# Optimization experiments

Hardware: AMD Instinct MI355X
Metric: run time of the kernel (lower is better)

## Reference

```python
import jax, jax.numpy as jnp
import numpy as np

N = 2_000_000           # agents
T = 10                  # timesteps
G_HOUSEHOLD = 800_000   # groups per edge type
G_COMPANY = 20_000
G_SCHOOL = 65_000
TAU = 0.1               # gumbel-softmax temperature (GradABM-JUNE default)


def setup_inputs() -> dict:
    key = jax.random.key(0)
    ks = jax.random.split(key, 6)
    # pre-sampled standard Gumbel noise for the differentiable Bernoulli sampling
    u = jax.random.uniform(ks[0], (T, 2, N), minval=1e-9, maxval=1.0)
    gumbel = (-jnp.log(-jnp.log(u))).astype(jnp.float32)
    return {
        "beta_parameters": jnp.array([0.3, 0.2, 0.4], dtype=jnp.float32),
        "transmissions": 0.1 * jax.random.uniform(ks[1], (N,), dtype=jnp.float32),
        "susceptibilities": jnp.ones((N,), dtype=jnp.float32),
        "gumbel": gumbel,
        "g_household": jax.random.randint(ks[2], (N,), 0, G_HOUSEHOLD),
        "g_company": jax.random.randint(ks[3], (N,), 0, G_COMPANY),
        "g_school": jax.random.randint(ks[4], (N,), 0, G_SCHOOL),
        "n_timesteps": T,
    }


def _infection_step(betas, transm, susc, gumbel_t, group_ids, group_sizes):
    """One InfectionPassing forward + gumbel-softmax sampling."""
    trans_susc = jnp.zeros_like(transm)
    for beta, gids, G in zip(betas, group_ids, group_sizes):
        # group sizes -> contact probability (constant wrt params)
        people = jax.ops.segment_sum(jnp.ones_like(transm), gids, num_segments=G)
        p_contact = jax.lax.stop_gradient(jnp.minimum(1.0 / (people - 1.0), 1.0))
        # agent -> group scatter-add of transmissions, weighted by beta * p_contact
        cum_trans = beta * p_contact * jax.ops.segment_sum(transm, gids, num_segments=G)
        # group -> agent gather, weighted by susceptibility
        trans_susc = trans_susc + cum_trans[gids] * susc
    not_infected = jnp.exp(-trans_susc)
    # hard (straight-through) gumbel-softmax Bernoulli sample, class 1 = infected
    logits = jnp.log(jnp.clip(jnp.stack([not_infected, 1.0 - not_infected]), 1e-15))  # [2, N]
    y = jax.nn.softmax((logits + gumbel_t) / TAU, axis=0)
    hard = jax.nn.one_hot(jnp.argmax(y, axis=0), 2, axis=0, dtype=y.dtype)
    sample = hard + y - jax.lax.stop_gradient(y)
    return sample[1]


def reference(beta_parameters, transmissions, susceptibilities, gumbel,
              g_household, g_company, g_school, n_timesteps):
    group_ids = (g_household, g_company, g_school)
    group_sizes = (G_HOUSEHOLD, G_COMPANY, G_SCHOOL)
    betas = (beta_parameters[0], beta_parameters[1], beta_parameters[2])

    def scan_fn(carry, gumbel_t):
        transm, susc = carry
        new_inf = _infection_step(betas, transm, susc, gumbel_t, group_ids, group_sizes)
        return (transm + 0.2 * new_inf, susc - new_inf), new_inf

    _, ret = jax.lax.scan(scan_fn, (transmissions, susceptibilities), gumbel[:n_timesteps])
    return ret  # [T, N] stacked new_infected per timestep (vstack equivalent)
```

## Files before the change

### kernel.cpp

```cpp
#include <hip/hip_runtime.h>

#define NAGENTS 2000000
#define GH 800000
#define GC 20000
#define GS 65000
#define GT (GH + GC + GS)
#define TSTEPS 10
#define NXCD 8

#define FIXD   17592186044416.0
#define INVFIX (1.0 / 17592186044416.0)
#define DELTA  3518437208883ULL
#define CUNIT  (1ULL << 51)
#define SMASK  (CUNIT - 1ULL)

#define SUSCBIT (1ULL << 63)

__global__ void init_pack_repl_kernel(const float* __restrict__ transm_in,
                                      const float* __restrict__ susc_in,
                                      const int* __restrict__ gh,
                                      const int* __restrict__ gc,
                                      const int* __restrict__ gs,
                                      unsigned long long* __restrict__ repl,
                                      unsigned long long* __restrict__ packed,
                                      int n) {
    int i = blockIdx.x * blockDim.x + threadIdx.x;
    if (i >= n) return;

    unsigned xcd;
    asm volatile("s_getreg_b32 %0, hwreg(HW_REG_XCC_ID)" : "=s"(xcd));
    unsigned long long* myrep = repl + (size_t)(xcd & (NXCD - 1)) * GT;

    int a = __builtin_nontemporal_load(&gh[i]);
    int b = __builtin_nontemporal_load(&gc[i]);
    int c = __builtin_nontemporal_load(&gs[i]);
    float sv = __builtin_nontemporal_load(&susc_in[i]);
    float tv = __builtin_nontemporal_load(&transm_in[i]);

    unsigned long long w = (unsigned long long)(unsigned)a
                         | ((unsigned long long)(unsigned)b << 20)
                         | ((unsigned long long)(unsigned)c << 35)
                         | (sv != 0.0f ? SUSCBIT : 0ULL);
    __builtin_nontemporal_store(w, &packed[i]);

    unsigned long long e =
        (unsigned long long)((double)tv * FIXD + 0.5) + CUNIT;
    __hip_atomic_fetch_add(&myrep[a], e, __ATOMIC_RELAXED,
                           __HIP_MEMORY_SCOPE_WORKGROUP);
    __hip_atomic_fetch_add(&myrep[GH + b], e, __ATOMIC_RELAXED,
                           __HIP_MEMORY_SCOPE_WORKGROUP);
    __hip_atomic_fetch_add(&myrep[GH + GC + c], e, __ATOMIC_RELAXED,
                           __HIP_MEMORY_SCOPE_WORKGROUP);
}

__global__ void combine_from_repl_kernel(const float* __restrict__ betas,
                                         const unsigned long long* __restrict__ repl,
                                         unsigned long long* __restrict__ buf,
                                         float* __restrict__ cur, int ntot) {
    int g = blockIdx.x * blockDim.x + threadIdx.x;
    if (g >= ntot) return;
    unsigned long long v = 0;
#pragma unroll
    for (int x = 0; x < NXCD; ++x)
        v += __builtin_nontemporal_load(&repl[(size_t)x * GT + g]);
    buf[g] = v;
    float people = (float)(v >> 51);
    float p = fminf(1.0f / (people - 1.0f), 1.0f);
    float beta = (g < GH) ? betas[0] : (g < GH + GC) ? betas[1] : betas[2];
    float sum = (float)((double)(long long)(v & SMASK) * INVFIX);
    cur[g] = (beta * p) * sum;
}

__global__ void combine_kernel(const float* __restrict__ betas,
                               const unsigned long long* __restrict__ buf,
                               float* __restrict__ cur, int ntot) {
    int g = blockIdx.x * blockDim.x + threadIdx.x;
    if (g >= ntot) return;
    unsigned long long v = __builtin_nontemporal_load(&buf[g]);
    float people = (float)(v >> 51);
    float p = fminf(1.0f / (people - 1.0f), 1.0f);
    float beta = (g < GH) ? betas[0] : (g < GH + GC) ? betas[1] : betas[2];
    float sum = (float)((double)(long long)(v & SMASK) * INVFIX);
    cur[g] = (beta * p) * sum;
}

template <bool LAST>
__global__ void step_packed_kernel(const float* __restrict__ gum_t,
                                   unsigned long long* __restrict__ packed,
                                   const float* __restrict__ cur,
                                   unsigned long long* __restrict__ buf,
                                   float* __restrict__ out_t,
                                   int n) {
    int i = blockIdx.x * blockDim.x + threadIdx.x;
    if (i >= n) return;

    unsigned long long w = __builtin_nontemporal_load(&packed[i]);
    float ninf = 0.0f;
    if (w & SUSCBIT) {
        int a = (int)(w & 0xFFFFFULL);
        int b = GH + (int)((w >> 20) & 0x7FFFULL);
        int c = GH + GC + (int)((w >> 35) & 0x1FFFFULL);
        float ts = cur[a];
        ts += cur[b];
        ts += cur[c];

        float ni = expf(-ts);
        float l0 = logf(fmaxf(ni, 1e-15f));
        float l1 = logf(fmaxf(1.0f - ni, 1e-15f));
        float g0 = __builtin_nontemporal_load(&gum_t[i]);
        float g1 = __builtin_nontemporal_load(&gum_t[(size_t)n + i]);
        float z0 = (l0 + g0) / 0.1f;
        float z1 = (l1 + g1) / 0.1f;
        if (z1 > z0) {
            ninf = 1.0f;
            if (!LAST) {
                packed[i] = w & ~SUSCBIT;
                atomicAdd(&buf[a], DELTA);
                atomicAdd(&buf[b], DELTA);
                atomicAdd(&buf[c], DELTA);
            }
        }
    }
    __builtin_nontemporal_store(ninf, &out_t[i]);
}

__global__ void init_pack_kernel(const float* __restrict__ transm_in,
                                 const float* __restrict__ susc_in,
                                 const int* __restrict__ gh,
                                 const int* __restrict__ gc,
                                 const int* __restrict__ gs,
                                 unsigned long long* __restrict__ buf,
                                 unsigned long long* __restrict__ packed,
                                 int n) {
    int i = blockIdx.x * blockDim.x + threadIdx.x;
    if (i >= n) return;
    int a = __builtin_nontemporal_load(&gh[i]);
    int b = __builtin_nontemporal_load(&gc[i]);
    int c = __builtin_nontemporal_load(&gs[i]);
    float sv = __builtin_nontemporal_load(&susc_in[i]);
    float tv = __builtin_nontemporal_load(&transm_in[i]);

    unsigned long long w = (unsigned long long)(unsigned)a
                         | ((unsigned long long)(unsigned)b << 20)
                         | ((unsigned long long)(unsigned)c << 35)
                         | (sv != 0.0f ? SUSCBIT : 0ULL);
    __builtin_nontemporal_store(w, &packed[i]);

    unsigned long long e =
        (unsigned long long)((double)tv * FIXD + 0.5) + CUNIT;
    atomicAdd(&buf[a], e);
    atomicAdd(&buf[GH + b], e);
    atomicAdd(&buf[GH + GC + c], e);
}

extern "C" void kernel_launch(void* const* d_in, const int* in_sizes, int n_in,
                              void* d_out, int out_size, void* d_ws, size_t ws_size,
                              hipStream_t stream) {
    const float* betas     = (const float*)d_in[0];
    const float* transm_in = (const float*)d_in[1];
    float*       susc      = (float*)d_in[2];
    const float* gumbel    = (const float*)d_in[3];
    const int*   gh        = (const int*)d_in[4];
    const int*   gc        = (const int*)d_in[5];
    const int*   gs        = (const int*)d_in[6];
    int          n         = in_sizes[1];
    float*       out       = (float*)d_out;

    unsigned long long* buf = (unsigned long long*)d_ws;
    float* cur = (float*)((char*)d_ws + (size_t)GT * 8);
    size_t packOff = ((size_t)GT * 12 + 255) & ~(size_t)255;
    unsigned long long* packed =
        (unsigned long long*)((char*)d_ws + packOff);
    size_t replOff = (packOff + (size_t)n * 8 + 255) & ~(size_t)255;
    unsigned long long* repl =
        (unsigned long long*)((char*)d_ws + replOff);
    size_t need_repl = replOff + (size_t)NXCD * GT * 8;
    size_t need_pack = packOff + (size_t)n * 8;

    const int blk = 256;
    const int grid_n = (n + blk - 1) / blk;
    const int grid_g = (GT + blk - 1) / blk;

    if (ws_size >= need_repl) {
        hipMemsetAsync(repl, 0, (size_t)NXCD * GT * 8, stream);
        init_pack_repl_kernel<<<grid_n, blk, 0, stream>>>(
            transm_in, susc, gh, gc, gs, repl, packed, n);
        for (int t = 0; t < TSTEPS; ++t) {
            const float* gum_t = gumbel + (size_t)2 * t * n;
            float* out_t = out + (size_t)t * n;
            if (t == 0) {
                combine_from_repl_kernel<<<grid_g, blk, 0, stream>>>(
                    betas, repl, buf, cur, GT);
            } else {
                combine_kernel<<<grid_g, blk, 0, stream>>>(betas, buf, cur, GT);
            }
            if (t == TSTEPS - 1) {
                step_packed_kernel<true><<<grid_n, blk, 0, stream>>>(
                    gum_t, packed, cur, buf, out_t, n);
            } else {
                step_packed_kernel<false><<<grid_n, blk, 0, stream>>>(
                    gum_t, packed, cur, buf, out_t, n);
            }
        }
        return;
    }

    hipMemsetAsync(buf, 0, (size_t)GT * 8, stream);
    if (ws_size >= need_pack) {
        init_pack_kernel<<<grid_n, blk, 0, stream>>>(
            transm_in, susc, gh, gc, gs, buf, packed, n);
        for (int t = 0; t < TSTEPS; ++t) {
            const float* gum_t = gumbel + (size_t)2 * t * n;
            float* out_t = out + (size_t)t * n;
            combine_kernel<<<grid_g, blk, 0, stream>>>(betas, buf, cur, GT);
            if (t == TSTEPS - 1) {
                step_packed_kernel<true><<<grid_n, blk, 0, stream>>>(
                    gum_t, packed, cur, buf, out_t, n);
            } else {
                step_packed_kernel<false><<<grid_n, blk, 0, stream>>>(
                    gum_t, packed, cur, buf, out_t, n);
            }
        }
    }
}
```

Before: 984.1 us.

## Replace per-XCD atomic scatter with binned counting-sort segment reduction

The initial group-sum scatter now uses a two-pass counting sort instead of per-XCD replicated global atomics. Agents are histogrammed into group-range bins per block, the histogram is prefix-scanned, (group, transmission) pairs are scattered into bins, and each bin is reduced with shared-memory atomics. The aim is to replace random global 64-bit atomics with LDS atomics and more local writes. The cost is extra passes, a 3N-entry binned buffer, several more kernel launches, and scatter writes with poor coalescing.

```diff
diff --git a/kernel.cpp b/kernel.cpp
--- a/kernel.cpp
+++ b/kernel.cpp
@@ -1,4 +1,6 @@
 #include <hip/hip_runtime.h>
+
+typedef unsigned long long u64;
 
 #define NAGENTS 2000000
 #define GH 800000
@@ -6,7 +8,6 @@
 #define GS 65000
 #define GT (GH + GC + GS)
 #define TSTEPS 10
-#define NXCD 8
 
 #define FIXD   17592186044416.0
 #define INVFIX (1.0 / 17592186044416.0)
@@ -16,54 +17,131 @@
 
 #define SUSCBIT (1ULL << 63)
 
-__global__ void init_pack_repl_kernel(const float* __restrict__ transm_in,
-                                      const float* __restrict__ susc_in,
-                                      const int* __restrict__ gh,
-                                      const int* __restrict__ gc,
-                                      const int* __restrict__ gs,
-                                      unsigned long long* __restrict__ repl,
-                                      unsigned long long* __restrict__ packed,
-                                      int n) {
-    int i = blockIdx.x * blockDim.x + threadIdx.x;
-    if (i >= n) return;
-
-    unsigned xcd;
-    asm volatile("s_getreg_b32 %0, hwreg(HW_REG_XCC_ID)" : "=s"(xcd));
-    unsigned long long* myrep = repl + (size_t)(xcd & (NXCD - 1)) * GT;
-
-    int a = __builtin_nontemporal_load(&gh[i]);
-    int b = __builtin_nontemporal_load(&gc[i]);
-    int c = __builtin_nontemporal_load(&gs[i]);
-    float sv = __builtin_nontemporal_load(&susc_in[i]);
-    float tv = __builtin_nontemporal_load(&transm_in[i]);
-
-    unsigned long long w = (unsigned long long)(unsigned)a
-                         | ((unsigned long long)(unsigned)b << 20)
-                         | ((unsigned long long)(unsigned)c << 35)
-                         | (sv != 0.0f ? SUSCBIT : 0ULL);
-    __builtin_nontemporal_store(w, &packed[i]);
-
-    unsigned long long e =
-        (unsigned long long)((double)tv * FIXD + 0.5) + CUNIT;
-    __hip_atomic_fetch_add(&myrep[a], e, __ATOMIC_RELAXED,
-                           __HIP_MEMORY_SCOPE_WORKGROUP);
-    __hip_atomic_fetch_add(&myrep[GH + b], e, __ATOMIC_RELAXED,
-                           __HIP_MEMORY_SCOPE_WORKGROUP);
-    __hip_atomic_fetch_add(&myrep[GH + GC + c], e, __ATOMIC_RELAXED,
-                           __HIP_MEMORY_SCOPE_WORKGROUP);
-}
-
-__global__ void combine_from_repl_kernel(const float* __restrict__ betas,
-                                         const unsigned long long* __restrict__ repl,
-                                         unsigned long long* __restrict__ buf,
-                                         float* __restrict__ cur, int ntot) {
+#define NB_H 3125
+#define NB_C 2500
+#define NB_S 2032
+#define NBINS (NB_H + NB_C + NB_S)
+#define NBP 256
+#define P12_THR 512
+#define SCAN_ELEMS 2048
+
+__device__ __forceinline__ int bin_h(int a) { return a >> 8; }
+__device__ __forceinline__ int bin_c(int c) { return NB_H + (c >> 3); }
+__device__ __forceinline__ int bin_s(int s) { return NB_H + NB_C + (s >> 5); }
+
+__global__ __launch_bounds__(P12_THR) void p1_hist_pack(
+    const int* __restrict__ gh, const int* __restrict__ gc,
+    const int* __restrict__ gs, const float* __restrict__ susc_in,
+    u64* __restrict__ packed, unsigned* __restrict__ hist,
+    int n, int apb) {
+    __shared__ unsigned h[NBINS];
+    for (int j = threadIdx.x; j < NBINS; j += P12_THR) h[j] = 0;
+    __syncthreads();
+    const int b = blockIdx.x;
+    const int lo = b * apb, hi = min(n, lo + apb);
+    for (int i = lo + threadIdx.x; i < hi; i += P12_THR) {
+        int a = gh[i], c = gc[i], s = gs[i];
+        float sv = susc_in[i];
+        u64 w = (u64)(unsigned)a | ((u64)(unsigned)c << 20)
+              | ((u64)(unsigned)s << 35) | (sv != 0.0f ? SUSCBIT : 0ULL);
+        __builtin_nontemporal_store(w, &packed[i]);
+        atomicAdd(&h[bin_h(a)], 1u);
+        atomicAdd(&h[bin_c(c)], 1u);
+        atomicAdd(&h[bin_s(s)], 1u);
+    }
+    __syncthreads();
+    for (int j = threadIdx.x; j < NBINS; j += P12_THR)
+        hist[(size_t)j * NBP + b] = h[j];
+}
+
+__global__ __launch_bounds__(1024) void s1_scan(unsigned* __restrict__ data,
+                                                unsigned* __restrict__ sums,
+                                                int ntot) {
+    __shared__ unsigned sA[1024], sB[1024];
+    const int base = blockIdx.x * SCAN_ELEMS;
+    const int t = threadIdx.x;
+    unsigned v0 = (base + 2 * t     < ntot) ? data[base + 2 * t]     : 0u;
+    unsigned v1 = (base + 2 * t + 1 < ntot) ? data[base + 2 * t + 1] : 0u;
+    sA[t] = v0 + v1;
+    __syncthreads();
+    unsigned* src = sA; unsigned* dst = sB;
+    for (int off = 1; off < 1024; off <<= 1) {
+        dst[t] = src[t] + (t >= off ? src[t - off] : 0u);
+        __syncthreads();
+        unsigned* tmp = src; src = dst; dst = tmp;
+    }
+    unsigned incl = src[t];
+    unsigned expair = incl - (v0 + v1);
+    if (base + 2 * t     < ntot) data[base + 2 * t]     = expair;
+    if (base + 2 * t + 1 < ntot) data[base + 2 * t + 1] = expair + v0;
+    if (t == 1023) sums[blockIdx.x] = incl;
+}
+
+__global__ __launch_bounds__(1024) void s3_add(unsigned* __restrict__ data,
+                                               const unsigned* __restrict__ exsums,
+                                               int ntot) {
+    unsigned base = exsums[blockIdx.x];
+    for (int k = 0; k < 2; ++k) {
+        int j = blockIdx.x * SCAN_ELEMS + k * 1024 + threadIdx.x;
+        if (j < ntot) data[j] += base;
+    }
+}
+
+__global__ __launch_bounds__(P12_THR) void p2_scatter(
+    const int* __restrict__ gh, const int* __restrict__ gc,
+    const int* __restrict__ gs, const float* __restrict__ transm,
+    const unsigned* __restrict__ offs, u64* __restrict__ binned,
+    int n, int apb) {
+    __shared__ unsigned cur[NBINS];
+    const int b = blockIdx.x;
+    for (int j = threadIdx.x; j < NBINS; j += P12_THR)
+        cur[j] = offs[(size_t)j * NBP + b];
+    __syncthreads();
+    const int lo = b * apb, hi = min(n, lo + apb);
+    for (int i = lo + threadIdx.x; i < hi; i += P12_THR) {
+        int a = gh[i], c = gc[i], s = gs[i];
+        unsigned fb = __float_as_uint(transm[i]);
+        unsigned r0 = atomicAdd(&cur[bin_h(a)], 1u);
+        binned[r0] = ((u64)(unsigned)a << 32) | fb;
+        unsigned r1 = atomicAdd(&cur[bin_c(c)], 1u);
+        binned[r1] = ((u64)(unsigned)(GH + c) << 32) | fb;
+        unsigned r2 = atomicAdd(&cur[bin_s(s)], 1u);
+        binned[r2] = ((u64)(unsigned)(GH + GC + s) << 32) | fb;
+    }
+}
+
+__global__ __launch_bounds__(256) void p3_reduce(
+    const unsigned* __restrict__ offs, const u64* __restrict__ binned,
+    u64* __restrict__ buf, int etotal) {
+    __shared__ u64 acc[256];
+    const int bin = blockIdx.x;
+    int gidbase, span;
+    if (bin < NB_H)               { gidbase = bin << 8;                      span = 256; }
+    else if (bin < NB_H + NB_C)   { gidbase = GH + ((bin - NB_H) << 3);      span = 8; }
+    else { gidbase = GH + GC + ((bin - NB_H - NB_C) << 5); span = min(32, GT - gidbase); }
+    for (int j = threadIdx.x; j < span; j += 256) acc[j] = 0ULL;
+    __syncthreads();
+    unsigned start = offs[(size_t)bin * NBP];
+    unsigned end = (bin == NBINS - 1) ? (unsigned)etotal
+                                      : offs[(size_t)(bin + 1) * NBP];
+    for (unsigned e = start + threadIdx.x; e < end; e += 256) {
+        u64 kv = binned[e];
+        int gid = (int)(kv >> 32);
+        float tv = __uint_as_float((unsigned)kv);
+        u64 ev = (u64)((double)tv * FIXD + 0.5) + CUNIT;
+        atomicAdd(&acc[gid - gidbase], ev);
+    }
+    __syncthreads();
+    for (int j = threadIdx.x; j < span; j += 256)
+        buf[gidbase + j] = acc[j];
+}
+
+__global__ void combine_kernel(const float* __restrict__ betas,
+                               const u64* __restrict__ buf,
+                               float* __restrict__ cur, int ntot) {
     int g = blockIdx.x * blockDim.x + threadIdx.x;
     if (g >= ntot) return;
-    unsigned long long v = 0;
-#pragma unroll
-    for (int x = 0; x < NXCD; ++x)
-        v += __builtin_nontemporal_load(&repl[(size_t)x * GT + g]);
-    buf[g] = v;
+    u64 v = __builtin_nontemporal_load(&buf[g]);
     float people = (float)(v >> 51);
     float p = fminf(1.0f / (people - 1.0f), 1.0f);
     float beta = (g < GH) ? betas[0] : (g < GH + GC) ? betas[1] : betas[2];
@@ -71,30 +149,17 @@
     cur[g] = (beta * p) * sum;
 }
 
-__global__ void combine_kernel(const float* __restrict__ betas,
-                               const unsigned long long* __restrict__ buf,
-                               float* __restrict__ cur, int ntot) {
-    int g = blockIdx.x * blockDim.x + threadIdx.x;
-    if (g >= ntot) return;
-    unsigned long long v = __builtin_nontemporal_load(&buf[g]);
-    float people = (float)(v >> 51);
-    float p = fminf(1.0f / (people - 1.0f), 1.0f);
-    float beta = (g < GH) ? betas[0] : (g < GH + GC) ? betas[1] : betas[2];
-    float sum = (float)((double)(long long)(v & SMASK) * INVFIX);
-    cur[g] = (beta * p) * sum;
-}
-
 template <bool LAST>
 __global__ void step_packed_kernel(const float* __restrict__ gum_t,
-                                   unsigned long long* __restrict__ packed,
+                                   u64* __restrict__ packed,
                                    const float* __restrict__ cur,
-                                   unsigned long long* __restrict__ buf,
+                                   u64* __restrict__ buf,
                                    float* __restrict__ out_t,
                                    int n) {
     int i = blockIdx.x * blockDim.x + threadIdx.x;
     if (i >= n) return;
 
-    unsigned long long w = __builtin_nontemporal_load(&packed[i]);
+    u64 w = __builtin_nontemporal_load(&packed[i]);
     float ninf = 0.0f;
     if (w & SUSCBIT) {
         int a = (int)(w & 0xFFFFFULL);
@@ -129,25 +194,18 @@
                                  const int* __restrict__ gh,
                                  const int* __restrict__ gc,
                                  const int* __restrict__ gs,
-                                 unsigned long long* __restrict__ buf,
-                                 unsigned long long* __restrict__ packed,
+                                 u64* __restrict__ buf,
+                                 u64* __restrict__ packed,
                                  int n) {
     int i = blockIdx.x * blockDim.x + threadIdx.x;
     if (i >= n) return;
-    int a = __builtin_nontemporal_load(&gh[i]);
-    int b = __builtin_nontemporal_load(&gc[i]);
-    int c = __builtin_nontemporal_load(&gs[i]);
-    float sv = __builtin_nontemporal_load(&susc_in[i]);
-    float tv = __builtin_nontemporal_load(&transm_in[i]);
-
-    unsigned long long w = (unsigned long long)(unsigned)a
-                         | ((unsigned long long)(unsigned)b << 20)
-                         | ((unsigned long long)(unsigned)c << 35)
-                         | (sv != 0.0f ? SUSCBIT : 0ULL);
+    int a = gh[i], b = gc[i], c = gs[i];
+    float sv = susc_in[i];
+    float tv = transm_in[i];
+    u64 w = (u64)(unsigned)a | ((u64)(unsigned)b << 20)
+          | ((u64)(unsigned)c << 35) | (sv != 0.0f ? SUSCBIT : 0ULL);
     __builtin_nontemporal_store(w, &packed[i]);
-
-    unsigned long long e =
-        (unsigned long long)((double)tv * FIXD + 0.5) + CUNIT;
+    u64 e = (u64)((double)tv * FIXD + 0.5) + CUNIT;
     atomicAdd(&buf[a], e);
     atomicAdd(&buf[GH + b], e);
     atomicAdd(&buf[GH + GC + c], e);
@@ -166,34 +224,42 @@
     int          n         = in_sizes[1];
     float*       out       = (float*)d_out;
 
-    unsigned long long* buf = (unsigned long long*)d_ws;
-    float* cur = (float*)((char*)d_ws + (size_t)GT * 8);
+    char* base = (char*)d_ws;
+    u64*   buf    = (u64*)base;
+    float* cur    = (float*)(base + (size_t)GT * 8);
     size_t packOff = ((size_t)GT * 12 + 255) & ~(size_t)255;
-    unsigned long long* packed =
-        (unsigned long long*)((char*)d_ws + packOff);
-    size_t replOff = (packOff + (size_t)n * 8 + 255) & ~(size_t)255;
-    unsigned long long* repl =
-        (unsigned long long*)((char*)d_ws + replOff);
-    size_t need_repl = replOff + (size_t)NXCD * GT * 8;
+    u64*   packed = (u64*)(base + packOff);
+    size_t binOff  = (packOff + (size_t)n * 8 + 255) & ~(size_t)255;
+    u64*   binned = (u64*)(base + binOff);
+    size_t histOff = (binOff + (size_t)3 * n * 8 + 255) & ~(size_t)255;
+    unsigned* hist = (unsigned*)(base + histOff);
+    size_t sumsOff = (histOff + (size_t)NBINS * NBP * 4 + 255) & ~(size_t)255;
+    unsigned* sums = (unsigned*)(base + sumsOff);
+    size_t need_sort = sumsOff + 4096;
     size_t need_pack = packOff + (size_t)n * 8;
 
     const int blk = 256;
     const int grid_n = (n + blk - 1) / blk;
     const int grid_g = (GT + blk - 1) / blk;
 
-    if (ws_size >= need_repl) {
-        hipMemsetAsync(repl, 0, (size_t)NXCD * GT * 8, stream);
-        init_pack_repl_kernel<<<grid_n, blk, 0, stream>>>(
-            transm_in, susc, gh, gc, gs, repl, packed, n);
+    if (ws_size >= need_sort) {
+        const int apb = (n + NBP - 1) / NBP;
+        const int nscan = NBINS * NBP;
+        const int nS1 = (nscan + SCAN_ELEMS - 1) / SCAN_ELEMS;
+
+        p1_hist_pack<<<NBP, P12_THR, 0, stream>>>(gh, gc, gs, susc,
+                                                  packed, hist, n, apb);
+        s1_scan<<<nS1, 1024, 0, stream>>>(hist, sums, nscan);
+        s1_scan<<<1, 1024, 0, stream>>>(sums, &sums[1023], nS1);
+        s3_add<<<nS1, 1024, 0, stream>>>(hist, sums, nscan);
+        p2_scatter<<<NBP, P12_THR, 0, stream>>>(gh, gc, gs, transm_in,
+                                                hist, binned, n, apb);
+        p3_reduce<<<NBINS, 256, 0, stream>>>(hist, binned, buf, 3 * n);
+
         for (int t = 0; t < TSTEPS; ++t) {
             const float* gum_t = gumbel + (size_t)2 * t * n;
             float* out_t = out + (size_t)t * n;
-            if (t == 0) {
-                combine_from_repl_kernel<<<grid_g, blk, 0, stream>>>(
-                    betas, repl, buf, cur, GT);
-            } else {
-                combine_kernel<<<grid_g, blk, 0, stream>>>(betas, buf, cur, GT);
-            }
+            combine_kernel<<<grid_g, blk, 0, stream>>>(betas, buf, cur, GT);
             if (t == TSTEPS - 1) {
                 step_packed_kernel<true><<<grid_n, blk, 0, stream>>>(
                     gum_t, packed, cur, buf, out_t, n);
```

Measured after the change: 904.4 us. 1.09x faster.
